# Performance work log

Hardware: AMD Instinct MI355X
Metric: run time of the kernel (lower is better)

The kernel has to match this reference:

```python
import jax, jax.numpy as jnp
import numpy as np

DN = ('NCHW', 'OIHW', 'NCHW')


def conv(x, w, s, p):
    return jax.lax.conv_general_dilated(x, w, (s, s), [(p, p), (p, p)], dimension_numbers=DN)


def batchnorm(x, g, b, eps=1e-5):
    # torch BatchNorm2d in training mode: biased batch stats over (N,H,W)
    mu = jnp.mean(x, (0, 2, 3), keepdims=True)
    var = jnp.var(x, (0, 2, 3), keepdims=True)
    return (x - mu) * jax.lax.rsqrt(var + eps) * g.reshape(1, -1, 1, 1) + b.reshape(1, -1, 1, 1)


def pconv(x, mask, W, b, s, p, gb, act):
    # PartialConvLayer.forward
    k = W.shape[-1]
    y = conv(x * mask, W, s, p)
    mc = conv(mask, jnp.ones((1, 1, k, k), x.dtype), s, p)  # all-ones mask conv (frozen)
    zero = mc == 0
    msum = jnp.where(zero, 1.0, mc)
    if b is not None:
        bias = b.reshape(1, -1, 1, 1)
        y = (y - bias) / msum + bias
    else:
        y = y / msum
    y = jnp.where(zero, 0.0, y)
    new_mask = jnp.where(zero, 0.0, 1.0).astype(x.dtype)
    if gb is not None:
        y = batchnorm(y, gb[0], gb[1])
    if act == 'relu':
        y = jax.nn.relu(y)
    elif act == 'leaky':
        y = jnp.where(y >= 0, y, 0.2 * y)
    return y, new_mask


def nlm(mask, feat, h2):
    # Vectorized batch_NLM: Nadaraya-Watson estimator between miss and bkg pixels.
    # Equivalent to the original triple loop: for each miss pixel i,
    #   out[i] = sum_j exp(-||x_i-x_j||^2/h^2) x_j / sum_j exp(-...)   over bkg j.
    # Subtracting the per-row min distance before exp is mathematically identical
    # (the factor cancels in the ratio) and numerically stable.
    bs, C, H, W = feat.shape
    N = H * W
    x = feat.transpose(0, 2, 3, 1).reshape(bs, N, C)
    bkg = mask.reshape(bs, N) > 0.5
    sq = jnp.sum(x * x, -1)  # [bs,N]
    D = jnp.maximum(sq[:, :, None] + sq[:, None, :] - 2.0 * jnp.einsum('bic,bjc->bij', x, x), 0.0)
    Dm = jnp.where(bkg[:, None, :], D, jnp.inf)
    dmin = jnp.min(Dm, -1, keepdims=True)
    w = jnp.where(bkg[:, None, :], jnp.exp(-(D - dmin) / h2), 0.0)
    avg = jnp.einsum('bij,bjc->bic', w, x) / jnp.sum(w, -1, keepdims=True)
    out = jnp.where(bkg[:, :, None], x, avg)  # only miss pixels are replaced
    return out.reshape(bs, H, W, C).transpose(0, 3, 1, 2)


def up2(x):
    return jnp.repeat(jnp.repeat(x, 2, axis=2), 2, axis=3)


def forward(input_x, mask, enc1_W, enc2_W, enc3_W, enc4_W, dec4_W, dec3_W, dec2_W, dec1_W, dec1_b,
            enc2_g, enc2_b, enc3_g, enc3_b, enc4_g, enc4_b,
            dec4_g, dec4_b, dec3_g, dec3_b, dec2_g, dec2_b):
    H_GAUSS2 = 25.0  # h_gaussian = 5
    h0, m0 = input_x, mask
    h1, m1 = pconv(h0, m0, enc1_W, None, 2, 3, None, 'relu')                 # down-7, bn=False
    h2, m2 = pconv(h1, m1, enc2_W, None, 2, 2, (enc2_g, enc2_b), 'relu')     # down-5
    # NLM feature swapping at layer 2 (torch code detaches -> stop_gradient)
    h2 = jax.lax.stop_gradient(nlm(m2, h2, H_GAUSS2))
    buffer_swapped = h2
    h3, m3 = pconv(h2, m2, enc3_W, None, 2, 1, (enc3_g, enc3_b), 'relu')     # down-3
    h4, m4 = pconv(h3, m3, enc4_W, None, 2, 1, (enc4_g, enc4_b), 'relu')     # down-3

    out, omask = h4, m4
    out, omask = up2(out), up2(omask)
    out, omask = pconv(jnp.concatenate([out, h3], 1), omask, dec4_W, None, 1, 1, (dec4_g, dec4_b), 'leaky')
    out, omask = up2(out), up2(omask)
    out, omask = pconv(jnp.concatenate([out, buffer_swapped], 1), omask, dec3_W, None, 1, 1, (dec3_g, dec3_b), 'leaky')
    out, omask = up2(out), up2(omask)
    out, omask = pconv(jnp.concatenate([out, h1], 1), omask, dec2_W, None, 1, 1, (dec2_g, dec2_b), 'leaky')
    out, omask = up2(out), up2(omask)
    out, omask = pconv(jnp.concatenate([out, h0], 1), omask, dec1_W, dec1_b, 1, 1, None, 'none')  # bn=False, bias, no act
    return out


def setup_inputs() -> dict:
    key = jax.random.key(0)
    ks = jax.random.split(key, 12)

    def kaiming(k, shape):
        fan_in = shape[1] * shape[2] * shape[3]
        return jax.random.normal(k, shape, jnp.float32) * np.float32(np.sqrt(2.0 / fan_in))

    bs = 8
    input_x = jax.random.normal(ks[0], (bs, 128, 144, 144), jnp.float32)
    # mask: 1 = background (valid), 0 = missing. Hole large enough to survive two downsamples.
    mask = jnp.ones((bs, 1, 144, 144), jnp.float32).at[:, :, 40:96, 40:96].set(0.0)

    inp = {
        'input_x': input_x,
        'mask': mask,
        'enc1_W': kaiming(ks[1], (256, 128, 7, 7)),
        'enc2_W': kaiming(ks[2], (512, 256, 5, 5)),
        'enc3_W': kaiming(ks[3], (512, 512, 3, 3)),
        'enc4_W': kaiming(ks[4], (512, 512, 3, 3)),
        'dec4_W': kaiming(ks[5], (512, 1024, 3, 3)),
        'dec3_W': kaiming(ks[6], (512, 1024, 3, 3)),
        'dec2_W': kaiming(ks[7], (256, 768, 3, 3)),
        'dec1_W': kaiming(ks[8], (128, 384, 3, 3)),
        'dec1_b': jnp.zeros((128,), jnp.float32),
    }
    for name, c in [('enc2', 512), ('enc3', 512), ('enc4', 512), ('dec4', 512), ('dec3', 512), ('dec2', 256)]:
        inp[name + '_g'] = jnp.ones((c,), jnp.float32)
        inp[name + '_b'] = jnp.zeros((c,), jnp.float32)
    return inp


def reference(input_x, mask, enc1_W, enc2_W, enc3_W, enc4_W, dec4_W, dec3_W, dec2_W, dec1_W, dec1_b,
              enc2_g, enc2_b, enc3_g, enc3_b, enc4_g, enc4_b,
              dec4_g, dec4_b, dec3_g, dec3_b, dec2_g, dec2_b):
    return forward(input_x, mask, enc1_W, enc2_W, enc3_W, enc4_W, dec4_W, dec3_W, dec2_W, dec1_W, dec1_b,
                   enc2_g, enc2_b, enc3_g, enc3_b, enc4_g, enc4_b,
                   dec4_g, dec4_b, dec3_g, dec3_b, dec2_g, dec2_b)
```

## Files before the change

kernel.cpp:

```cpp
#include <hip/hip_runtime.h>
#include <math.h>

#define ACT_NONE 0
#define ACT_RELU 1
#define ACT_LEAKY 2

#define EPI_F32 0
#define EPI_PAIR_RELU 1
#define EPI_F32_BIAS 2

typedef __attribute__((ext_vector_type(8))) short short8;
typedef __attribute__((ext_vector_type(8))) __bf16 bf16x8;
typedef __attribute__((ext_vector_type(4))) float f32x4;
typedef __attribute__((ext_vector_type(4))) unsigned uint4v;

__device__ __forceinline__ float actf(float y, int act) {
    if (act == ACT_RELU)  return y > 0.f ? y : 0.f;
    if (act == ACT_LEAKY) return y >= 0.f ? y : 0.2f * y;
    return y;
}

__device__ __forceinline__ unsigned f2bf_rne(float f) {
    unsigned u = __float_as_uint(f);
    return (u + 0x7FFFu + ((u >> 16) & 1u)) >> 16;
}
__device__ __forceinline__ float bf2f(unsigned h) { return __uint_as_float(h << 16); }
__device__ __forceinline__ unsigned splitpack(float f) {
    unsigned hi = f2bf_rne(f);
    float r = f - bf2f(hi);
    unsigned lo = f2bf_rne(r);
    return (hi & 0xFFFFu) | (lo << 16);
}

__device__ __forceinline__ f32x4 mfma16(short8 a, short8 b, f32x4 c) {
    return __builtin_amdgcn_mfma_f32_16x16x32_bf16(
        __builtin_bit_cast(bf16x8, a), __builtin_bit_cast(bf16x8, b), c, 0, 0, 0);
}

template<int K, int S, bool MHALF>
__global__ void maskconv_kernel(const float* __restrict__ M, int HM, int WM,
                                float* __restrict__ mc, float* __restrict__ nm,
                                int N, int Hin, int Win, int Hout, int Wout) {
    constexpr int P = (K - 1) / 2;
    int idx = blockIdx.x * blockDim.x + threadIdx.x;
    int total = N * Hout * Wout;
    if (idx >= total) return;
    int wo = idx % Wout;
    int t  = idx / Wout;
    int ho = t % Hout;
    int n  = t / Hout;
    float s = 0.f;
    for (int kh = 0; kh < K; ++kh) {
        int ih = ho * S - P + kh;
        if ((unsigned)ih >= (unsigned)Hin) continue;
        const float* mrow = M + ((size_t)n * HM + (MHALF ? (ih >> 1) : ih)) * WM;
        for (int kw = 0; kw < K; ++kw) {
            int iw = wo * S - P + kw;
            if ((unsigned)iw < (unsigned)Win)
                s += mrow[MHALF ? (iw >> 1) : iw];
        }
    }
    mc[idx] = s;
    nm[idx] = (s == 0.f) ? 0.f : 1.f;
}

__global__ void wtransform(const float* __restrict__ W, short* __restrict__ Whi,
                           short* __restrict__ Wlo, int Cout, int Cin, int Ksz,
                           size_t total) {
    size_t idx = (size_t)blockIdx.x * blockDim.x + threadIdx.x;
    if (idx >= total) return;
    int j = (int)(idx & 7);
    int lane = (int)((idx >> 3) & 63);
    size_t r = idx >> 9;
    int COB = Cout >> 4, KB = Cin >> 5;
    int cob = (int)(r % COB); r /= COB;
    int kb = (int)(r % KB);
    int tap = (int)(r / KB);
    int co = cob * 16 + (lane & 15);
    int ci = kb * 32 + (lane >> 4) * 8 + j;
    float f = W[((size_t)co * Cin + ci) * Ksz + tap];
    unsigned hi = f2bf_rne(f);
    float rr = f - bf2f(hi);
    unsigned lo = f2bf_rne(rr);
    Whi[idx] = (short)hi;
    Wlo[idx] = (short)lo;
}

template<int K, int S, int TH, int TW, int NFW, bool AF32, int EPI>
__global__ __launch_bounds__(512) void conv_enc(
    const void* __restrict__ Asrc, int Cin, int Hin, int Win,
    const float* __restrict__ M,
    const short* __restrict__ Whi, const short* __restrict__ Wlo,
    const float* __restrict__ mc, const float* __restrict__ bias,
    void* __restrict__ outp,
    int Hout, int Wout, int Cout, int TX)
{
    static_assert(S == 2, "parity layout assumes stride 2");
    constexpr int P = (K - 1) / 2;
    constexpr int HH  = (TH - 1) * S + K;
    constexpr int HWC = (TW - 1) * S + K;
    constexpr int PXC = HH * HWC;
    static_assert(PXC <= 512, "one halo pixel per thread");
    constexpr int PW  = (HWC + 1) / 2;
    constexpr int PXC2 = HH * PW * 2;
    __shared__ __align__(16) unsigned BH[4 * PXC2 * 4];
    __shared__ __align__(16) unsigned BL[4 * PXC2 * 4];

    const int t    = threadIdx.x;
    const int lane = t & 63;
    const int wv   = t >> 6;
    const int wm   = wv >> 1;
    const int wn   = wv & 1;
    const int img  = blockIdx.z;
    const int coB  = blockIdx.y * 256;
    const int tile = blockIdx.x;
    const int ty   = tile / TX, tx = tile - ty * TX;
    const int oy0  = ty * TH, ox0 = tx * TW;
    const int KB   = Cin >> 5;
    const int COB  = Cout >> 4;
    const size_t HW = (size_t)Hin * Win;
    const int g  = lane >> 4;
    const int pl = lane & 15;

    bool sel = false;
    size_t base = 0;
    int qq = 0;
    if (t < PXC) {
        const int r = t / HWC, c = t - r * HWC;
        qq = r * PW + (c >> 1) + (c & 1) * (HH * PW);
        const int iy = oy0 * S - P + r;
        const int ix = ox0 * S - P + c;
        if ((unsigned)iy < (unsigned)Hin && (unsigned)ix < (unsigned)Win) {
            if (M[(size_t)img * HW + (size_t)iy * Win + ix] != 0.f) {
                sel = true;
                base = (size_t)img * Cin * HW + (size_t)iy * Win + ix;
            }
        }
    }

    unsigned vr[4][8];
    auto prefetch = [&](int kb) {
#pragma unroll
        for (int gg = 0; gg < 4; ++gg) {
            const int c0 = kb * 32 + gg * 8;
#pragma unroll
            for (int j = 0; j < 8; ++j) vr[gg][j] = 0u;
            if (sel) {
                const unsigned* s = (const unsigned*)Asrc + base + (size_t)c0 * HW;
#pragma unroll
                for (int j = 0; j < 8; ++j) vr[gg][j] = s[(size_t)j * HW];
            }
        }
    };

    f32x4 acc[4][NFW] = {};
    if (t < PXC) prefetch(0);

#pragma unroll 1
    for (int kb = 0; kb < KB; ++kb) {
        if (t < PXC) {
#pragma unroll
            for (int gg = 0; gg < 4; ++gg) {
                unsigned v[8];
#pragma unroll
                for (int j = 0; j < 8; ++j) {
                    v[j] = vr[gg][j];
                    if (AF32) v[j] = splitpack(__uint_as_float(v[j]));
                }
                uint4v hd, ld;
#pragma unroll
                for (int j = 0; j < 4; ++j) {
                    hd[j] = (v[2 * j] & 0xFFFFu) | (v[2 * j + 1] << 16);
                    ld[j] = (v[2 * j] >> 16) | (v[2 * j + 1] & 0xFFFF0000u);
                }
                *(uint4v*)&BH[(gg * PXC2 + qq) * 4] = hd;
                *(uint4v*)&BL[(gg * PXC2 + qq) * 4] = ld;
            }
        }
        __syncthreads();
        if (t < PXC && kb + 1 < KB) prefetch(kb + 1);

#pragma unroll 1
        for (int kh = 0; kh < K; ++kh)
#pragma unroll 1
        for (int kw = 0; kw < K; ++kw) {
            const int tap = kh * K + kw;
            const size_t wb = (((size_t)tap * KB + kb) * COB + (coB >> 4) + wm * 4) * 512
                            + (size_t)lane * 8;
            short8 ah[4], al[4];
#pragma unroll
            for (int fm = 0; fm < 4; ++fm) {
                ah[fm] = *(const short8*)(Whi + wb + (size_t)fm * 512);
                al[fm] = *(const short8*)(Wlo + wb + (size_t)fm * 512);
            }
#pragma unroll
            for (int fn = 0; fn < NFW; ++fn) {
                const int pxf = (wn * NFW + fn) * 16 + pl;
                const int oy = pxf / TW, ox = pxf - oy * TW;
                const int q2 = (oy * S + kh) * PW + ox + (kw >> 1) + (kw & 1) * (HH * PW);
                short8 bh = *(const short8*)&BH[(g * PXC2 + q2) * 4];
                short8 bl = *(const short8*)&BL[(g * PXC2 + q2) * 4];
#pragma unroll
                for (int fm = 0; fm < 4; ++fm) {
                    acc[fm][fn] = mfma16(ah[fm], bh, acc[fm][fn]);
                    acc[fm][fn] = mfma16(al[fm], bh, acc[fm][fn]);
                    acc[fm][fn] = mfma16(ah[fm], bl, acc[fm][fn]);
                }
            }
        }
        __syncthreads();
    }

    const int Npix = Hout * Wout;
    const float* mcb = mc + (size_t)img * Npix;
#pragma unroll
    for (int fm = 0; fm < 4; ++fm)
#pragma unroll
    for (int fn = 0; fn < NFW; ++fn) {
        const int co = coB + (wm * 4 + fm) * 16 + (lane >> 4) * 4;
        const int pxf = (wn * NFW + fn) * 16 + (lane & 15);
        const int oy = pxf / TW, ox = pxf - oy * TW;
        const int gy = oy0 + oy, gx = ox0 + ox;
        if (gy >= Hout || gx >= Wout) continue;
        const float m = mcb[(size_t)gy * Wout + gx];
        f32x4 a = acc[fm][fn];
#pragma unroll
        for (int r = 0; r < 4; ++r) {
            float y = a[r];
            if (EPI == EPI_F32_BIAS) {
                const float bv = bias[co + r];
                y = (m == 0.f) ? 0.f : (y - bv) / m + bv;
            } else {
                y = (m == 0.f) ? 0.f : y / m;
            }
            const size_t oidx = ((size_t)img * Cout + co + r) * Npix + (size_t)gy * Wout + gx;
            if (EPI == EPI_PAIR_RELU) {
                y = y > 0.f ? y : 0.f;
                ((unsigned*)outp)[oidx] = splitpack(y);
            } else {
                ((float*)outp)[oidx] = y;
            }
        }
    }
}

template<int TH, int TW, int NFW, bool BF32, int EPI>
__global__ __launch_bounds__(512) void conv3x3(
    const void* __restrict__ Asrc, int CA, int HA, int WA,
    const void* __restrict__ Bsrc, int CB,
    const float* __restrict__ M,
    const short* __restrict__ Whi, const short* __restrict__ Wlo,
    const float* __restrict__ mc, const float* __restrict__ bias,
    void* __restrict__ outp,
    int Hout, int Wout, int Cout, int TX)
{
    constexpr int HALO_H = TH + 2, HALO_W = TW + 2, HALO = HALO_H * HALO_W;
    constexpr int NPIX = TH * TW;
    constexpr int SITER = (HALO + 127) / 128;
    static_assert(NPIX == 32 * NFW, "tile must be exactly 32*NFW pixels");
    __shared__ __align__(16) unsigned BH[4 * HALO * 4];
    __shared__ __align__(16) unsigned BL[4 * HALO * 4];

    const int t    = threadIdx.x;
    const int lane = t & 63;
    const int wv   = t >> 6;
    const int wm   = wv >> 1;
    const int wn   = wv & 1;
    const int img  = blockIdx.z;
    const int coB  = blockIdx.y * 128;
    const int tile = blockIdx.x;
    const int ty   = tile / TX;
    const int tx   = tile - ty * TX;
    const int oy0  = ty * TH, ox0 = tx * TW;
    const int Cin  = CA + CB;
    const int KB   = Cin >> 5;
    const int COB  = Cout >> 4;
    const int WM   = Wout >> 1;
    const size_t HWA = (size_t)HA * WA;
    const size_t HWB = (size_t)Hout * Wout;

    const int sg = t >> 7;
    const int st = t & 127;
    const int g  = lane >> 4;
    const int pl = lane & 15;

    bool ssel[SITER];
    size_t sA[SITER], sB[SITER];
#pragma unroll
    for (int i = 0; i < SITER; ++i) {
        ssel[i] = false; sA[i] = 0; sB[i] = 0;
        const int q = st + i * 128;
        if (q < HALO) {
            const int hy = q / HALO_W, hx = q - hy * HALO_W;
            const int iy = oy0 - 1 + hy, ix = ox0 - 1 + hx;
            if ((unsigned)iy < (unsigned)Hout && (unsigned)ix < (unsigned)Wout) {
                if (M[((size_t)img * (Hout >> 1) + (iy >> 1)) * WM + (ix >> 1)] != 0.f) {
                    ssel[i] = true;
                    sA[i] = (size_t)img * CA * HWA + (size_t)(iy >> 1) * WA + (ix >> 1);
                    sB[i] = (size_t)img * CB * HWB + (size_t)iy * Wout + ix;
                }
            }
        }
    }

    unsigned vr[SITER][8];
    auto prefetch = [&](int kb) {
        const int c = kb * 32 + sg * 8;
#pragma unroll
        for (int i = 0; i < SITER; ++i) {
            const int q = st + i * 128;
#pragma unroll
            for (int j = 0; j < 8; ++j) vr[i][j] = 0u;
            if (q < HALO && ssel[i]) {
                if (c < CA) {
                    const unsigned* s = (const unsigned*)Asrc + sA[i] + (size_t)c * HWA;
#pragma unroll
                    for (int j = 0; j < 8; ++j) vr[i][j] = s[(size_t)j * HWA];
                } else {
                    const unsigned* s = (const unsigned*)Bsrc + sB[i] + (size_t)(c - CA) * HWB;
#pragma unroll
                    for (int j = 0; j < 8; ++j) vr[i][j] = s[(size_t)j * HWB];
                }
            }
        }
    };

    f32x4 acc[2][NFW] = {};
    const size_t wstride = (size_t)KB * COB * 512;
    prefetch(0);

#pragma unroll 1
    for (int kb = 0; kb < KB; ++kb) {
        const bool isB = (kb * 32 + sg * 8) >= CA;
#pragma unroll
        for (int i = 0; i < SITER; ++i) {
            const int q = st + i * 128;
            if (q < HALO) {
                unsigned v[8];
#pragma unroll
                for (int j = 0; j < 8; ++j) {
                    v[j] = vr[i][j];
                    if (BF32 && isB) v[j] = splitpack(__uint_as_float(v[j]));
                }
                uint4v hd, ld;
#pragma unroll
                for (int j = 0; j < 4; ++j) {
                    hd[j] = (v[2 * j] & 0xFFFFu) | (v[2 * j + 1] << 16);
                    ld[j] = (v[2 * j] >> 16) | (v[2 * j + 1] & 0xFFFF0000u);
                }
                *(uint4v*)&BH[(sg * HALO + q) * 4] = hd;
                *(uint4v*)&BL[(sg * HALO + q) * 4] = ld;
            }
        }
        __syncthreads();
        if (kb + 1 < KB) prefetch(kb + 1);

        size_t wb = ((size_t)kb * COB + (coB >> 4) + wm * 2) * 512 + (size_t)lane * 8;
#pragma unroll 1
        for (int tap = 0; tap < 9; ++tap) {
            const int dh = tap / 3, dw = tap - dh * 3;
            short8 ah0 = *(const short8*)(Whi + wb);
            short8 ah1 = *(const short8*)(Whi + wb + 512);
            short8 al0 = *(const short8*)(Wlo + wb);
            short8 al1 = *(const short8*)(Wlo + wb + 512);
#pragma unroll
            for (int fn = 0; fn < NFW; ++fn) {
                const int pxf = (wn * NFW + fn) * 16 + pl;
                const int oy = pxf / TW, ox = pxf - oy * TW;
                const int hpx = (oy + dh) * HALO_W + (ox + dw);
                short8 bh = *(const short8*)&BH[(g * HALO + hpx) * 4];
                short8 bl = *(const short8*)&BL[(g * HALO + hpx) * 4];
                acc[0][fn] = mfma16(ah0, bh, acc[0][fn]);
                acc[1][fn] = mfma16(ah1, bh, acc[1][fn]);
                acc[0][fn] = mfma16(al0, bh, acc[0][fn]);
                acc[1][fn] = mfma16(al1, bh, acc[1][fn]);
                acc[0][fn] = mfma16(ah0, bl, acc[0][fn]);
                acc[1][fn] = mfma16(ah1, bl, acc[1][fn]);
            }
            wb += wstride;
        }
        __syncthreads();
    }

    const float* mcb = mc + (size_t)img * HWB;
#pragma unroll
    for (int fm = 0; fm < 2; ++fm)
#pragma unroll
    for (int fn = 0; fn < NFW; ++fn) {
        const int co = coB + (wm * 2 + fm) * 16 + (lane >> 4) * 4;
        const int pxf = (wn * NFW + fn) * 16 + (lane & 15);
        const int oy = pxf / TW, ox = pxf - oy * TW;
        const int gy = oy0 + oy, gx = ox0 + ox;
        if (gy >= Hout || gx >= Wout) continue;
        const float m = mcb[(size_t)gy * Wout + gx];
        f32x4 a = acc[fm][fn];
#pragma unroll
        for (int r = 0; r < 4; ++r) {
            float y = a[r];
            if (EPI == EPI_F32_BIAS) {
                const float bv = bias[co + r];
                y = (m == 0.f) ? 0.f : (y - bv) / m + bv;
            } else {
                y = (m == 0.f) ? 0.f : y / m;
            }
            ((float*)outp)[((size_t)img * Cout + co + r) * HWB + (size_t)gy * Wout + gx] = y;
        }
    }
}

__global__ __launch_bounds__(256) void bn_stats_kernel(const float* __restrict__ y,
                                                       int N, int C, int HW,
                                                       float* __restrict__ mean,
                                                       float* __restrict__ istd) {
    const int c = blockIdx.x;
    double s = 0.0, s2 = 0.0;
    const int tot = N * HW;
    for (int i = threadIdx.x; i < tot; i += blockDim.x) {
        int n = i / HW, hw = i - n * HW;
        float v = y[((size_t)n * C + c) * HW + hw];
        s += v;
        s2 += (double)v * v;
    }
    __shared__ double sh[256], sh2[256];
    sh[threadIdx.x] = s; sh2[threadIdx.x] = s2;
    __syncthreads();
    for (int o = 128; o > 0; o >>= 1) {
        if (threadIdx.x < o) { sh[threadIdx.x] += sh[threadIdx.x + o]; sh2[threadIdx.x] += sh2[threadIdx.x + o]; }
        __syncthreads();
    }
    if (threadIdx.x == 0) {
        double mu = sh[0] / tot;
        double var = sh2[0] / tot - mu * mu;
        mean[c] = (float)mu;
        istd[c] = (float)(1.0 / sqrt(var + 1e-5));
    }
}

__global__ void bn_apply_pair(const float* __restrict__ y,
                              const float* __restrict__ mean, const float* __restrict__ istd,
                              const float* __restrict__ g, const float* __restrict__ b,
                              unsigned* __restrict__ pout, float* __restrict__ fout,
                              int C, int HW, int total, int act) {
    int idx = blockIdx.x * blockDim.x + threadIdx.x;
    if (idx >= total) return;
    int c = (idx / HW) % C;
    float v = (y[idx] - mean[c]) * istd[c] * g[c] + b[c];
    v = actf(v, act);
    pout[idx] = splitpack(v);
    if (fout) fout[idx] = v;
}

#define NLM_C 512
#define NLM_N 1296
#define NLM_MAXM 256
#define NLM_RT 16
#define NLM_KB1 16
#define NLM_KB2 41
#define NLM_PFRAG (NLM_KB1 * NLM_RT * 512)
#define NLM_WFRAG (NLM_KB2 * NLM_RT * 512)

__global__ __launch_bounds__(256) void nlm_trans(const float* __restrict__ h2f,
                                                 unsigned* __restrict__ xTp) {
    __shared__ float tile[32][33];
    const int b = blockIdx.z;
    const int j0 = blockIdx.x * 32, c0 = blockIdx.y * 32;
    const int tx = threadIdx.x & 31, ty = threadIdx.x >> 5;
    for (int cc = ty; cc < 32; cc += 8) {
        const int j = j0 + tx;
        tile[cc][tx] = (j < NLM_N) ? h2f[((size_t)b * NLM_C + c0 + cc) * NLM_N + j] : 0.f;
    }
    __syncthreads();
    for (int jj = ty; jj < 32; jj += 8) {
        const int j = j0 + jj;
        if (j < NLM_N)
            xTp[((size_t)b * NLM_N + j) * NLM_C + c0 + tx] = splitpack(tile[tx][jj]);
    }
}

__global__ void nlm_sq2(const float* __restrict__ h2f, float* __restrict__ sq) {
    const int b = blockIdx.y;
    const int j = blockIdx.x * 256 + threadIdx.x;
    if (j >= NLM_N) return;
    const float* p = h2f + (size_t)b * NLM_C * NLM_N + j;
    float s0 = 0.f, s1 = 0.f, s2 = 0.f, s3 = 0.f;
    for (int c = 0; c < NLM_C; c += 4) {
        float v0 = p[(size_t)c * NLM_N];
        float v1 = p[(size_t)(c + 1) * NLM_N];
        float v2 = p[(size_t)(c + 2) * NLM_N];
        float v3 = p[(size_t)(c + 3) * NLM_N];
        s0 = fmaf(v0, v0, s0); s1 = fmaf(v1, v1, s1);
        s2 = fmaf(v2, v2, s2); s3 = fmaf(v3, v3, s3);
    }
    sq[b * NLM_N + j] = (s0 + s1) + (s2 + s3);
}

__global__ void nlm_compact(const float* __restrict__ nm2, int* __restrict__ list,
                            int* __restrict__ cnt) {
    const int b = blockIdx.x;
    for (int j = threadIdx.x; j < NLM_N; j += 256) {
        if (nm2[(size_t)b * NLM_N + j] == 0.f) {
            int pos = atomicAdd(&cnt[b], 1);
            if (pos < NLM_MAXM) list[b * NLM_MAXM + pos] = j;
        }
    }
}

__global__ void nlm_gather(const unsigned* __restrict__ xTp, const int* __restrict__ list,
                           const int* __restrict__ cnt,
                           short* __restrict__ Phi, short* __restrict__ Plo) {
    const int b = blockIdx.y;
    const int id = blockIdx.x * 256 + threadIdx.x;
    const int i  = id >> 6;
    const int rem = id & 63;
    const int kb = rem >> 2, kg = rem & 3;
    const int lane = kg * 16 + (i & 15), rt = i >> 4;
    const size_t f = (size_t)b * NLM_PFRAG + ((size_t)(kb * NLM_RT + rt) * 64 + lane) * 8;
    if (i < cnt[b]) {
        const int pix = list[b * NLM_MAXM + i];
        const unsigned* s = xTp + ((size_t)b * NLM_N + pix) * NLM_C + kb * 32 + kg * 8;
#pragma unroll
        for (int jj = 0; jj < 8; ++jj) {
            unsigned v = s[jj];
            Phi[f + jj] = (short)(v & 0xFFFFu);
            Plo[f + jj] = (short)(v >> 16);
        }
    } else {
#pragma unroll
        for (int jj = 0; jj < 8; ++jj) { Phi[f + jj] = 0; Plo[f + jj] = 0; }
    }
}

__global__ __launch_bounds__(512) void nlm_gemm1(
    const unsigned* __restrict__ xTp, const short* __restrict__ Phi,
    const short* __restrict__ Plo, const int* __restrict__ cnt,
    float* __restrict__ S) {
    const int img = blockIdx.z, mt = blockIdx.y, nt = blockIdx.x;
    if (mt * 128 >= cnt[img]) return;
    __shared__ __align__(16) unsigned BH[4 * 128 * 4];
    __shared__ __align__(16) unsigned BL[4 * 128 * 4];
    const int t = threadIdx.x, lane = t & 63, wv = t >> 6, wm = wv >> 1, wn = wv & 1;
    const int j0 = nt * 128;
    const int spx = t & 127, sg = t >> 7;
    f32x4 acc[2][4] = {};
#pragma unroll 1
    for (int kb = 0; kb < NLM_KB1; ++kb) {
        unsigned v[8];
#pragma unroll
        for (int jj = 0; jj < 8; ++jj) v[jj] = 0u;
        const int j = j0 + spx;
        if (j < NLM_N) {
            const unsigned* s = xTp + ((size_t)img * NLM_N + j) * NLM_C + kb * 32 + sg * 8;
#pragma unroll
            for (int jj = 0; jj < 8; ++jj) v[jj] = s[jj];
        }
        uint4v hd, ld;
#pragma unroll
        for (int jj = 0; jj < 4; ++jj) {
            hd[jj] = (v[2 * jj] & 0xFFFFu) | (v[2 * jj + 1] << 16);
            ld[jj] = (v[2 * jj] >> 16) | (v[2 * jj + 1] & 0xFFFF0000u);
        }
        *(uint4v*)&BH[(sg * 128 + spx) * 4] = hd;
        *(uint4v*)&BL[(sg * 128 + spx) * 4] = ld;
        __syncthreads();
        const size_t ab = (size_t)img * NLM_PFRAG
                        + (size_t)(kb * NLM_RT + mt * 8 + wm * 2) * 512 + (size_t)lane * 8;
        short8 ah0 = *(const short8*)(Phi + ab);
        short8 ah1 = *(const short8*)(Phi + ab + 512);
        short8 al0 = *(const short8*)(Plo + ab);
        short8 al1 = *(const short8*)(Plo + ab + 512);
        const int g = lane >> 4, pl = lane & 15;
#pragma unroll
        for (int fn = 0; fn < 4; ++fn) {
            const int px = wn * 64 + fn * 16 + pl;
            short8 bh = *(const short8*)&BH[(g * 128 + px) * 4];
            short8 bl = *(const short8*)&BL[(g * 128 + px) * 4];
            acc[0][fn] = mfma16(ah0, bh, acc[0][fn]);
            acc[1][fn] = mfma16(ah1, bh, acc[1][fn]);
            acc[0][fn] = mfma16(al0, bh, acc[0][fn]);
            acc[1][fn] = mfma16(al1, bh, acc[1][fn]);
            acc[0][fn] = mfma16(ah0, bl, acc[0][fn]);
            acc[1][fn] = mfma16(ah1, bl, acc[1][fn]);
        }
        __syncthreads();
    }
#pragma unroll
    for (int fm = 0; fm < 2; ++fm)
#pragma unroll
    for (int fn = 0; fn < 4; ++fn) {
        const int row = mt * 128 + (wm * 2 + fm) * 16 + (lane >> 4) * 4;
        const int j = j0 + wn * 64 + fn * 16 + (lane & 15);
        if (j >= NLM_N) continue;
        f32x4 a = acc[fm][fn];
#pragma unroll
        for (int r = 0; r < 4; ++r)
            S[((size_t)img * NLM_MAXM + row + r) * NLM_N + j] = a[r];
    }
}

__global__ __launch_bounds__(256) void nlm_row(
    const float* __restrict__ S, const float* __restrict__ sq,
    const float* __restrict__ nm2, const int* __restrict__ list,
    const int* __restrict__ cnt,
    short* __restrict__ W2hi, short* __restrict__ W2lo,
    float* __restrict__ sumw, float inv_h2) {
    const int img = blockIdx.y, i = blockIdx.x;
    if (i >= cnt[img] || i >= NLM_MAXM) return;
    __shared__ float Drow[NLM_N];
    __shared__ float red[256];
    const int tid = threadIdx.x;
    const int pix = list[img * NLM_MAXM + i];
    const float sqi = sq[img * NLM_N + pix];
    const float BIG = 3.4e38f;
    float lmin = BIG;
    for (int j = tid; j < NLM_N; j += 256) {
        float d = BIG;
        if (nm2[(size_t)img * NLM_N + j] != 0.f) {
            float dot = S[((size_t)img * NLM_MAXM + i) * NLM_N + j];
            d = sqi + sq[img * NLM_N + j] - 2.f * dot;
            d = d > 0.f ? d : 0.f;
            lmin = d < lmin ? d : lmin;
        }
        Drow[j] = d;
    }
    red[tid] = lmin;
    __syncthreads();
    for (int o = 128; o > 0; o >>= 1) {
        if (tid < o) red[tid] = fminf(red[tid], red[tid + o]);
        __syncthreads();
    }
    const float dmin = red[0];
    __syncthreads();

    const int rt = i >> 4, lr = i & 15;
    float lsum = 0.f;
    for (int j = tid; j < NLM_KB2 * 32; j += 256) {
        float w = 0.f;
        if (j < NLM_N && Drow[j] < 3.3e38f) {
            w = expf(-(Drow[j] - dmin) * inv_h2);
            lsum += w;
        }
        const unsigned u = splitpack(w);
        const int kb = j >> 5, kg = (j & 31) >> 3, jj = j & 7;
        const int lane = kg * 16 + lr;
        const size_t f = (size_t)img * NLM_WFRAG
                       + ((size_t)(kb * NLM_RT + rt) * 64 + lane) * 8 + jj;
        W2hi[f] = (short)(u & 0xFFFFu);
        W2lo[f] = (short)(u >> 16);
    }
    red[tid] = lsum;
    __syncthreads();
    for (int o = 128; o > 0; o >>= 1) {
        if (tid < o) red[tid] += red[tid + o];
        __syncthreads();
    }
    if (tid == 0) sumw[img * NLM_MAXM + i] = red[0];
}

__global__ __launch_bounds__(512) void nlm_gemm2(
    const unsigned* __restrict__ xTp, const short* __restrict__ W2hi,
    const short* __restrict__ W2lo, const int* __restrict__ cnt,
    const float* __restrict__ sumw, const int* __restrict__ list,
    unsigned* __restrict__ out) {
    const int img = blockIdx.z, mt = blockIdx.y, ct = blockIdx.x;
    const int cN = cnt[img] < NLM_MAXM ? cnt[img] : NLM_MAXM;
    if (mt * 128 >= cN) return;
    __shared__ __align__(16) unsigned BH[4 * 128 * 4];
    __shared__ __align__(16) unsigned BL[4 * 128 * 4];
    const int t = threadIdx.x, lane = t & 63, wv = t >> 6, wm = wv >> 1, wn = wv & 1;
    const int c0 = ct * 128;
    const int sc = t & 127, sg = t >> 7;
    f32x4 acc[2][4] = {};
#pragma unroll 1
    for (int kb = 0; kb < NLM_KB2; ++kb) {
        unsigned v[8];
#pragma unroll
        for (int jj = 0; jj < 8; ++jj) {
            const int j = kb * 32 + sg * 8 + jj;
            v[jj] = (j < NLM_N)
                  ? xTp[((size_t)img * NLM_N + j) * NLM_C + c0 + sc] : 0u;
        }
        uint4v hd, ld;
#pragma unroll
        for (int jj = 0; jj < 4; ++jj) {
            hd[jj] = (v[2 * jj] & 0xFFFFu) | (v[2 * jj + 1] << 16);
            ld[jj] = (v[2 * jj] >> 16) | (v[2 * jj + 1] & 0xFFFF0000u);
        }
        *(uint4v*)&BH[(sg * 128 + sc) * 4] = hd;
        *(uint4v*)&BL[(sg * 128 + sc) * 4] = ld;
        __syncthreads();
        const size_t ab = (size_t)img * NLM_WFRAG
                        + (size_t)(kb * NLM_RT + mt * 8 + wm * 2) * 512 + (size_t)lane * 8;
        short8 ah0 = *(const short8*)(W2hi + ab);
        short8 ah1 = *(const short8*)(W2hi + ab + 512);
        short8 al0 = *(const short8*)(W2lo + ab);
        short8 al1 = *(const short8*)(W2lo + ab + 512);
        const int g = lane >> 4, pl = lane & 15;
#pragma unroll
        for (int fn = 0; fn < 4; ++fn) {
            const int px = wn * 64 + fn * 16 + pl;
            short8 bh = *(const short8*)&BH[(g * 128 + px) * 4];
            short8 bl = *(const short8*)&BL[(g * 128 + px) * 4];
            acc[0][fn] = mfma16(ah0, bh, acc[0][fn]);
            acc[1][fn] = mfma16(ah1, bh, acc[1][fn]);
            acc[0][fn] = mfma16(al0, bh, acc[0][fn]);
            acc[1][fn] = mfma16(al1, bh, acc[1][fn]);
            acc[0][fn] = mfma16(ah0, bl, acc[0][fn]);
            acc[1][fn] = mfma16(ah1, bl, acc[1][fn]);
        }
        __syncthreads();
    }
#pragma unroll
    for (int fm = 0; fm < 2; ++fm)
#pragma unroll
    for (int fn = 0; fn < 4; ++fn) {
        const int row = mt * 128 + (wm * 2 + fm) * 16 + (lane >> 4) * 4;
        const int c = c0 + wn * 64 + fn * 16 + (lane & 15);
        f32x4 a = acc[fm][fn];
#pragma unroll
        for (int r = 0; r < 4; ++r) {
            const int ri = row + r;
            if (ri < cN) {
                const float y = a[r] / sumw[img * NLM_MAXM + ri];
                out[((size_t)img * NLM_C + c) * NLM_N + list[img * NLM_MAXM + ri]]
                    = splitpack(y);
            }
        }
    }
}

extern "C" void kernel_launch(void* const* d_in, const int* in_sizes, int n_in,
                              void* d_out, int out_size, void* d_ws, size_t ws_size,
                              hipStream_t stream) {
    const float* x0    = (const float*)d_in[0];
    const float* m0    = (const float*)d_in[1];
    const float* Wsrc[8] = {
        (const float*)d_in[2], (const float*)d_in[3], (const float*)d_in[4],
        (const float*)d_in[5], (const float*)d_in[6], (const float*)d_in[7],
        (const float*)d_in[8], (const float*)d_in[9]
    };
    const float* dec1b = (const float*)d_in[10];
    const float* enc2g = (const float*)d_in[11];
    const float* enc2b = (const float*)d_in[12];
    const float* enc3g = (const float*)d_in[13];
    const float* enc3b = (const float*)d_in[14];
    const float* enc4g = (const float*)d_in[15];
    const float* enc4b = (const float*)d_in[16];
    const float* dec4g = (const float*)d_in[17];
    const float* dec4b = (const float*)d_in[18];
    const float* dec3g = (const float*)d_in[19];
    const float* dec3b = (const float*)d_in[20];
    const float* dec2g = (const float*)d_in[21];
    const float* dec2b = (const float*)d_in[22];
    float* outp = (float*)d_out;

    const int N = 8;
    float* ws = (float*)d_ws;
    size_t off = 0;
    auto alloc = [&](size_t nf) {
        size_t o = off;
        off += ((nf + 63) / 64) * 64;
        return ws + o;
    };

    unsigned* h1pair  = (unsigned*)alloc(10616832);
    unsigned* h2spair = (unsigned*)alloc(5308416);
    unsigned* h3pair  = (unsigned*)alloc(1327104);
    unsigned* h4pair  = (unsigned*)alloc(331776);
    unsigned* d4pair  = (unsigned*)alloc(1327104);
    float* ybuf = alloc(10616832);
    float* h2f  = alloc(5308416);
    unsigned* xTp = (unsigned*)alloc(5308416);
    float* sqb  = alloc(10368);
    float* mc   = alloc(165888);
    float* nm1  = alloc(41472);
    float* nm2  = alloc(10368);
    float* nm3  = alloc(2592);
    float* nm4  = alloc(648);
    float* nmd4 = alloc(2592);
    float* nmd3 = alloc(10368);
    float* nmd2 = alloc(41472);
    float* nmx  = alloc(165888);
    float* bmean = alloc(512);
    float* bistd = alloc(512);
    short* Whi = (short*)alloc(10625024);
    short* Wlo = (short*)alloc(10625024);
    float* Smat = alloc((size_t)8 * NLM_MAXM * NLM_N);
    short* Phi  = (short*)alloc((size_t)8 * NLM_PFRAG / 2);
    short* Plo  = (short*)alloc((size_t)8 * NLM_PFRAG / 2);
    short* W2hi = (short*)alloc((size_t)8 * NLM_WFRAG / 2);
    short* W2lo = (short*)alloc((size_t)8 * NLM_WFRAG / 2);
    int*   mlist = (int*)alloc(8 * NLM_MAXM);
    int*   mcnt  = (int*)alloc(64);
    float* sumw  = alloc(8 * NLM_MAXM);
    unsigned* d3pair = h2spair;
    unsigned* d2pair = h1pair;

    if (ws_size < off * sizeof(float)) return;

    auto cdiv = [](size_t a, size_t b) { return (int)((a + b - 1) / b); };

    struct WLay { int Cout, Cin, K; size_t ofs; };
    const WLay WL[8] = {
        {256, 128, 7, 0},
        {512, 256, 5, 1605632},
        {512, 512, 3, 4882432},
        {512, 512, 3, 7241728},
        {512, 1024, 3, 9601024},
        {512, 1024, 3, 14319616},
        {256, 768, 3, 19038208},
        {128, 384, 3, 20807680},
    };
    for (int i = 0; i < 8; ++i) {
        size_t tot = (size_t)WL[i].Cout * WL[i].Cin * WL[i].K * WL[i].K;
        wtransform<<<cdiv(tot, 256), 256, 0, stream>>>(
            Wsrc[i], Whi + WL[i].ofs, Wlo + WL[i].ofs, WL[i].Cout, WL[i].Cin,
            WL[i].K * WL[i].K, tot);
    }

    maskconv_kernel<7, 2, false><<<cdiv(N * 72 * 72, 256), 256, 0, stream>>>(
        m0, 144, 144, mc, nm1, N, 144, 144, 72, 72);
    conv_enc<7, 2, 8, 8, 2, true, EPI_PAIR_RELU><<<dim3(81, 1, N), 512, 0, stream>>>(
        x0, 128, 144, 144, m0,
        Whi + WL[0].ofs, Wlo + WL[0].ofs, mc, nullptr, h1pair,
        72, 72, 256, 9);

    maskconv_kernel<5, 2, false><<<cdiv(N * 36 * 36, 256), 256, 0, stream>>>(
        nm1, 72, 72, mc, nm2, N, 72, 72, 36, 36);
    conv_enc<5, 2, 8, 8, 2, false, EPI_F32><<<dim3(25, 2, N), 512, 0, stream>>>(
        h1pair, 256, 72, 72, nm1,
        Whi + WL[1].ofs, Wlo + WL[1].ofs, mc, nullptr, ybuf,
        36, 36, 512, 5);
    bn_stats_kernel<<<512, 256, 0, stream>>>(ybuf, N, 512, 1296, bmean, bistd);
    bn_apply_pair<<<cdiv(5308416, 256), 256, 0, stream>>>(
        ybuf, bmean, bistd, enc2g, enc2b, h2spair, h2f, 512, 1296, 5308416, ACT_RELU);

    nlm_trans<<<dim3(41, 16, N), 256, 0, stream>>>(h2f, xTp);
    nlm_sq2<<<dim3(6, N), 256, 0, stream>>>(h2f, sqb);
    hipMemsetAsync(mcnt, 0, 8 * sizeof(int), stream);
    nlm_compact<<<N, 256, 0, stream>>>(nm2, mlist, mcnt);
    nlm_gather<<<dim3(64, N), 256, 0, stream>>>(xTp, mlist, mcnt, Phi, Plo);
    nlm_gemm1<<<dim3(11, 2, N), 512, 0, stream>>>(xTp, Phi, Plo, mcnt, Smat);
    nlm_row<<<dim3(NLM_MAXM, N), 256, 0, stream>>>(Smat, sqb, nm2, mlist, mcnt,
                                                   W2hi, W2lo, sumw, 1.f / 25.f);
    nlm_gemm2<<<dim3(4, 2, N), 512, 0, stream>>>(xTp, W2hi, W2lo, mcnt, sumw,
                                                 mlist, h2spair);

    maskconv_kernel<3, 2, false><<<cdiv(N * 18 * 18, 256), 256, 0, stream>>>(
        nm2, 36, 36, mc, nm3, N, 36, 36, 18, 18);
    conv_enc<3, 2, 4, 8, 1, false, EPI_F32><<<dim3(15, 2, N), 512, 0, stream>>>(
        h2spair, 512, 36, 36, nm2,
        Whi + WL[2].ofs, Wlo + WL[2].ofs, mc, nullptr, ybuf,
        18, 18, 512, 3);
    bn_stats_kernel<<<512, 256, 0, stream>>>(ybuf, N, 512, 324, bmean, bistd);
    bn_apply_pair<<<cdiv(1327104, 256), 256, 0, stream>>>(
        ybuf, bmean, bistd, enc3g, enc3b, h3pair, nullptr, 512, 324, 1327104, ACT_RELU);

    maskconv_kernel<3, 2, false><<<cdiv(N * 9 * 9, 256), 256, 0, stream>>>(
        nm3, 18, 18, mc, nm4, N, 18, 18, 9, 9);
    conv_enc<3, 2, 4, 8, 1, false, EPI_F32><<<dim3(6, 2, N), 512, 0, stream>>>(
        h3pair, 512, 18, 18, nm3,
        Whi + WL[3].ofs, Wlo + WL[3].ofs, mc, nullptr, ybuf,
        9, 9, 512, 2);
    bn_stats_kernel<<<512, 256, 0, stream>>>(ybuf, N, 512, 81, bmean, bistd);
    bn_apply_pair<<<cdiv(331776, 256), 256, 0, stream>>>(
        ybuf, bmean, bistd, enc4g, enc4b, h4pair, nullptr, 512, 81, 331776, ACT_RELU);

    maskconv_kernel<3, 1, true><<<cdiv(N * 18 * 18, 256), 256, 0, stream>>>(
        nm4, 9, 9, mc, nmd4, N, 18, 18, 18, 18);
    conv3x3<8, 8, 2, false, EPI_F32><<<dim3(9, 4, N), 512, 0, stream>>>(
        h4pair, 512, 9, 9, h3pair, 512, nm4,
        Whi + WL[4].ofs, Wlo + WL[4].ofs, mc, nullptr, ybuf,
        18, 18, 512, 3);
    bn_stats_kernel<<<512, 256, 0, stream>>>(ybuf, N, 512, 324, bmean, bistd);
    bn_apply_pair<<<cdiv(1327104, 256), 256, 0, stream>>>(
        ybuf, bmean, bistd, dec4g, dec4b, d4pair, nullptr, 512, 324, 1327104, ACT_LEAKY);

    maskconv_kernel<3, 1, true><<<cdiv(N * 36 * 36, 256), 256, 0, stream>>>(
        nmd4, 18, 18, mc, nmd3, N, 36, 36, 36, 36);
    conv3x3<8, 12, 3, false, EPI_F32><<<dim3(15, 4, N), 512, 0, stream>>>(
        d4pair, 512, 18, 18, h2spair, 512, nmd4,
        Whi + WL[5].ofs, Wlo + WL[5].ofs, mc, nullptr, ybuf,
        36, 36, 512, 3);
    bn_stats_kernel<<<512, 256, 0, stream>>>(ybuf, N, 512, 1296, bmean, bistd);
    bn_apply_pair<<<cdiv(5308416, 256), 256, 0, stream>>>(
        ybuf, bmean, bistd, dec3g, dec3b, d3pair, nullptr, 512, 1296, 5308416, ACT_LEAKY);

    maskconv_kernel<3, 1, true><<<cdiv(N * 72 * 72, 256), 256, 0, stream>>>(
        nmd3, 36, 36, mc, nmd2, N, 72, 72, 72, 72);
    conv3x3<8, 16, 4, false, EPI_F32><<<dim3(45, 2, N), 512, 0, stream>>>(
        d3pair, 512, 36, 36, h1pair, 256, nmd3,
        Whi + WL[6].ofs, Wlo + WL[6].ofs, mc, nullptr, ybuf,
        72, 72, 256, 5);
    bn_stats_kernel<<<256, 256, 0, stream>>>(ybuf, N, 256, 5184, bmean, bistd);
    bn_apply_pair<<<cdiv(10616832, 256), 256, 0, stream>>>(
        ybuf, bmean, bistd, dec2g, dec2b, d2pair, nullptr, 256, 5184, 10616832, ACT_LEAKY);

    maskconv_kernel<3, 1, true><<<cdiv(N * 144 * 144, 256), 256, 0, stream>>>(
        nmd2, 72, 72, mc, nmx, N, 144, 144, 144, 144);
    conv3x3<8, 16, 4, true, EPI_F32_BIAS><<<dim3(162, 1, N), 512, 0, stream>>>(
        d2pair, 256, 72, 72, x0, 128, nmd2,
        Whi + WL[7].ofs, Wlo + WL[7].ofs, mc, dec1b, outp,
        144, 144, 128, 9);
}
```

Before: 2.826 ms.

## Add 4-wave conv3x3 variant with 64-channel output tiles for dec2/dec1

```diff
diff --git a/kernel.cpp b/kernel.cpp
--- a/kernel.cpp
+++ b/kernel.cpp
@@ -355,7 +355,7 @@
         __syncthreads();
         if (kb + 1 < KB) prefetch(kb + 1);
 
-        size_t wb = ((size_t)kb * COB + (coB >> 4) + wm * 2) * 512 + (size_t)lane * 8;
+        size_t wb = ((size_t)kb * COB + (coB >> 4) + wm * 2) * 512 + lane * 8;
 #pragma unroll 1
         for (int tap = 0; tap < 9; ++tap) {
             const int dh = tap / 3, dw = tap - dh * 3;
@@ -389,6 +389,160 @@
     for (int fn = 0; fn < NFW; ++fn) {
         const int co = coB + (wm * 2 + fm) * 16 + (lane >> 4) * 4;
         const int pxf = (wn * NFW + fn) * 16 + (lane & 15);
+        const int oy = pxf / TW, ox = pxf - oy * TW;
+        const int gy = oy0 + oy, gx = ox0 + ox;
+        if (gy >= Hout || gx >= Wout) continue;
+        const float m = mcb[(size_t)gy * Wout + gx];
+        f32x4 a = acc[fm][fn];
+#pragma unroll
+        for (int r = 0; r < 4; ++r) {
+            float y = a[r];
+            if (EPI == EPI_F32_BIAS) {
+                const float bv = bias[co + r];
+                y = (m == 0.f) ? 0.f : (y - bv) / m + bv;
+            } else {
+                y = (m == 0.f) ? 0.f : y / m;
+            }
+            ((float*)outp)[((size_t)img * Cout + co + r) * HWB + (size_t)gy * Wout + gx] = y;
+        }
+    }
+}
+
+template<int TH, int TW, int NFW, bool BF32, int EPI>
+__global__ __launch_bounds__(256) void conv3x3_w4(
+    const void* __restrict__ Asrc, int CA, int HA, int WA,
+    const void* __restrict__ Bsrc, int CB,
+    const float* __restrict__ M,
+    const short* __restrict__ Whi, const short* __restrict__ Wlo,
+    const float* __restrict__ mc, const float* __restrict__ bias,
+    void* __restrict__ outp,
+    int Hout, int Wout, int Cout, int TX)
+{
+    constexpr int HALO_H = TH + 2, HALO_W = TW + 2, HALO = HALO_H * HALO_W;
+    constexpr int NPIX = TH * TW;
+    constexpr int SITER = (HALO + 63) / 64;
+    static_assert(NPIX == 64 * NFW, "tile must be exactly 64*NFW pixels");
+    __shared__ __align__(16) unsigned BH[4 * HALO * 4];
+    __shared__ __align__(16) unsigned BL[4 * HALO * 4];
+
+    const int t    = threadIdx.x;
+    const int lane = t & 63;
+    const int wv   = t >> 6;
+    const int img  = blockIdx.z;
+    const int coB  = blockIdx.y * 64;
+    const int tile = blockIdx.x;
+    const int ty   = tile / TX;
+    const int tx   = tile - ty * TX;
+    const int oy0  = ty * TH, ox0 = tx * TW;
+    const int Cin  = CA + CB;
+    const int KB   = Cin >> 5;
+    const int COB  = Cout >> 4;
+    const int WM   = Wout >> 1;
+    const size_t HWA = (size_t)HA * WA;
+    const size_t HWB = (size_t)Hout * Wout;
+    const int g  = lane >> 4;
+    const int pl = lane & 15;
+
+    bool ssel[SITER];
+    size_t sA[SITER], sB[SITER];
+#pragma unroll
+    for (int i = 0; i < SITER; ++i) {
+        ssel[i] = false; sA[i] = 0; sB[i] = 0;
+        const int q = lane + i * 64;
+        if (q < HALO) {
+            const int hy = q / HALO_W, hx = q - hy * HALO_W;
+            const int iy = oy0 - 1 + hy, ix = ox0 - 1 + hx;
+            if ((unsigned)iy < (unsigned)Hout && (unsigned)ix < (unsigned)Wout) {
+                if (M[((size_t)img * (Hout >> 1) + (iy >> 1)) * WM + (ix >> 1)] != 0.f) {
+                    ssel[i] = true;
+                    sA[i] = (size_t)img * CA * HWA + (size_t)(iy >> 1) * WA + (ix >> 1);
+                    sB[i] = (size_t)img * CB * HWB + (size_t)iy * Wout + ix;
+                }
+            }
+        }
+    }
+
+    f32x4 acc[4][NFW] = {};
+    const size_t wstride = (size_t)KB * COB * 512;
+
+#pragma unroll 1
+    for (int kb = 0; kb < KB; ++kb) {
+        {
+            const int c = kb * 32 + wv * 8;
+            const bool isA = c < CA;
+#pragma unroll
+            for (int i = 0; i < SITER; ++i) {
+                const int q = lane + i * 64;
+                if (q < HALO) {
+                    unsigned v[8];
+#pragma unroll
+                    for (int j = 0; j < 8; ++j) v[j] = 0u;
+                    if (ssel[i]) {
+                        if (isA) {
+                            const unsigned* s = (const unsigned*)Asrc + sA[i] + (size_t)c * HWA;
+#pragma unroll
+                            for (int j = 0; j < 8; ++j) v[j] = s[(size_t)j * HWA];
+                        } else {
+                            if (BF32) {
+                                const float* s = (const float*)Bsrc + sB[i] + (size_t)(c - CA) * HWB;
+#pragma unroll
+                                for (int j = 0; j < 8; ++j) v[j] = splitpack(s[(size_t)j * HWB]);
+                            } else {
+                                const unsigned* s = (const unsigned*)Bsrc + sB[i] + (size_t)(c - CA) * HWB;
+#pragma unroll
+                                for (int j = 0; j < 8; ++j) v[j] = s[(size_t)j * HWB];
+                            }
+                        }
+                    }
+                    uint4v hd, ld;
+#pragma unroll
+                    for (int j = 0; j < 4; ++j) {
+                        hd[j] = (v[2 * j] & 0xFFFFu) | (v[2 * j + 1] << 16);
+                        ld[j] = (v[2 * j] >> 16) | (v[2 * j + 1] & 0xFFFF0000u);
+                    }
+                    *(uint4v*)&BH[(wv * HALO + q) * 4] = hd;
+                    *(uint4v*)&BL[(wv * HALO + q) * 4] = ld;
+                }
+            }
+        }
+        __syncthreads();
+
+        size_t wb = ((size_t)kb * COB + (coB >> 4)) * 512 + (size_t)lane * 8;
+#pragma unroll 1
+        for (int tap = 0; tap < 9; ++tap) {
+            const int dh = tap / 3, dw = tap - dh * 3;
+            short8 ah[4], al[4];
+#pragma unroll
+            for (int fm = 0; fm < 4; ++fm) {
+                ah[fm] = *(const short8*)(Whi + wb + (size_t)fm * 512);
+                al[fm] = *(const short8*)(Wlo + wb + (size_t)fm * 512);
+            }
+#pragma unroll
+            for (int fn = 0; fn < NFW; ++fn) {
+                const int pxf = (wv * NFW + fn) * 16 + pl;
+                const int oy = pxf / TW, ox = pxf - oy * TW;
+                const int hpx = (oy + dh) * HALO_W + (ox + dw);
+                short8 bh = *(const short8*)&BH[(g * HALO + hpx) * 4];
+                short8 bl = *(const short8*)&BL[(g * HALO + hpx) * 4];
+#pragma unroll
+                for (int fm = 0; fm < 4; ++fm) {
+                    acc[fm][fn] = mfma16(ah[fm], bh, acc[fm][fn]);
+                    acc[fm][fn] = mfma16(al[fm], bh, acc[fm][fn]);
+                    acc[fm][fn] = mfma16(ah[fm], bl, acc[fm][fn]);
+                }
+            }
+            wb += wstride;
+        }
+        __syncthreads();
+    }
+
+    const float* mcb = mc + (size_t)img * HWB;
+#pragma unroll
+    for (int fm = 0; fm < 4; ++fm)
+#pragma unroll
+    for (int fn = 0; fn < NFW; ++fn) {
+        const int co = coB + fm * 16 + (lane >> 4) * 4;
+        const int pxf = (wv * NFW + fn) * 16 + (lane & 15);
         const int oy = pxf / TW, ox = pxf - oy * TW;
         const int gy = oy0 + oy, gx = ox0 + ox;
         if (gy >= Hout || gx >= Wout) continue;
@@ -887,17 +1041,17 @@
 
     maskconv_kernel<3, 1, true><<<cdiv(N * 72 * 72, 256), 256, 0, stream>>>(
         nmd3, 36, 36, mc, nmd2, N, 72, 72, 72, 72);
-    conv3x3<8, 16, 4, false, EPI_F32><<<dim3(45, 2, N), 512, 0, stream>>>(
+    conv3x3_w4<24, 8, 3, false, EPI_F32><<<dim3(27, 4, N), 256, 0, stream>>>(
         d3pair, 512, 36, 36, h1pair, 256, nmd3,
         Whi + WL[6].ofs, Wlo + WL[6].ofs, mc, nullptr, ybuf,
-        72, 72, 256, 5);
+        72, 72, 256, 9);
     bn_stats_kernel<<<256, 256, 0, stream>>>(ybuf, N, 256, 5184, bmean, bistd);
     bn_apply_pair<<<cdiv(10616832, 256), 256, 0, stream>>>(
         ybuf, bmean, bistd, dec2g, dec2b, d2pair, nullptr, 256, 5184, 10616832, ACT_LEAKY);
 
     maskconv_kernel<3, 1, true><<<cdiv(N * 144 * 144, 256), 256, 0, stream>>>(
         nmd2, 72, 72, mc, nmx, N, 144, 144, 144, 144);
-    conv3x3<8, 16, 4, true, EPI_F32_BIAS><<<dim3(162, 1, N), 512, 0, stream>>>(
+    conv3x3_w4<16, 16, 4, true, EPI_F32_BIAS><<<dim3(81, 2, N), 256, 0, stream>>>(
         d2pair, 256, 72, 72, x0, 128, nmd2,
         Whi + WL[7].ofs, Wlo + WL[7].ofs, mc, dec1b, outp,
         144, 144, 128, 9);
```

Measured after the change: 2.836 ms. No clear change (+0.4%).
